# Kernel tuning notes

Hardware: AMD Instinct MI355X
Metric: run time of the kernel (lower is better)

## Reference

```python
import jax, jax.numpy as jnp
import numpy as np

B, S, HID = 2, 2048, 1024
NH, NKV, HD = 16, 8, 128
EPS = 1e-6
THETA = 1.0e6
NEG = -1e9

def _rope_tables():
    inv_freq = 1.0 / (THETA ** (np.arange(0, HD, 2, dtype=np.float32) / HD))  # [HD/2]
    pos = np.arange(S, dtype=np.float32)
    freqs = np.outer(pos, inv_freq)                      # [S, HD/2]
    emb = np.concatenate([freqs, freqs], axis=-1)        # [S, HD]
    cos = np.broadcast_to(np.cos(emb), (B, S, HD)).copy()
    sin = np.broadcast_to(np.sin(emb), (B, S, HD)).copy()
    return jnp.asarray(cos), jnp.asarray(sin)

def setup_inputs() -> dict:
    key = jax.random.key(0)
    ks = jax.random.split(key, 8)
    hidden_states = jax.random.normal(ks[0], (B, S, HID), jnp.float32)
    cos, sin = _rope_tables()
    # additive causal mask [B,1,S,S]
    causal = jnp.triu(jnp.full((S, S), NEG, jnp.float32), k=1)
    attention_mask = jnp.broadcast_to(causal[None, None], (B, 1, S, S))
    std = 0.02
    Wq = jax.random.normal(ks[1], (NH * HD, HID), jnp.float32) * std
    Wk = jax.random.normal(ks[2], (NKV * HD, HID), jnp.float32) * std
    Wv = jax.random.normal(ks[3], (NKV * HD, HID), jnp.float32) * std
    Wo = jax.random.normal(ks[4], (HID, NH * HD), jnp.float32) * std
    q_norm_w = jnp.ones((HD,), jnp.float32)
    k_norm_w = jnp.ones((HD,), jnp.float32)
    return {"hidden_states": hidden_states, "cos": cos, "sin": sin,
            "attention_mask": attention_mask, "Wq": Wq, "Wk": Wk, "Wv": Wv,
            "Wo": Wo, "q_norm_w": q_norm_w, "k_norm_w": k_norm_w}

def _rms_norm(x, w):
    var = jnp.mean(jnp.square(x), axis=-1, keepdims=True)
    return x * jax.lax.rsqrt(var + EPS) * w

def _rotate_half(x):
    x1, x2 = jnp.split(x, 2, axis=-1)
    return jnp.concatenate([-x2, x1], axis=-1)

def reference(hidden_states, cos, sin, attention_mask, Wq, Wk, Wv, Wo, q_norm_w, k_norm_w):
    # projections: [B,S,heads,HD] -> [B,heads,S,HD]
    q = jnp.einsum('bsh,dh->bsd', hidden_states, Wq).reshape(B, S, NH, HD)
    k = jnp.einsum('bsh,dh->bsd', hidden_states, Wk).reshape(B, S, NKV, HD)
    v = jnp.einsum('bsh,dh->bsd', hidden_states, Wv).reshape(B, S, NKV, HD)
    q = jnp.transpose(_rms_norm(q, q_norm_w), (0, 2, 1, 3))
    k = jnp.transpose(_rms_norm(k, k_norm_w), (0, 2, 1, 3))
    v = jnp.transpose(v, (0, 2, 1, 3))
    c = cos[:, None]  # [B,1,S,HD]
    s = sin[:, None]
    q = q * c + _rotate_half(q) * s
    k = k * c + _rotate_half(k) * s
    # repeat kv heads: NKV -> NH
    n_rep = NH // NKV
    k = jnp.repeat(k, n_rep, axis=1)
    v = jnp.repeat(v, n_rep, axis=1)
    scaling = HD ** -0.5
    scores = jnp.einsum('bhqd,bhkd->bhqk', q, k) * scaling
    scores = scores + attention_mask
    probs = jax.nn.softmax(scores.astype(jnp.float32), axis=-1).astype(q.dtype)
    out = jnp.einsum('bhqk,bhkd->bhqd', probs, v)
    out = jnp.transpose(out, (0, 2, 1, 3)).reshape(B, S, NH * HD)
    return jnp.einsum('bsd,hd->bsh', out, Wo)
```

## Files before the change

### kernel.cpp

```cpp
#include <hip/hip_runtime.h>
#include <hip/hip_fp16.h>


typedef _Float16 f16;
typedef __attribute__((ext_vector_type(8))) _Float16 f16x8;
typedef __attribute__((ext_vector_type(4))) _Float16 f16x4;
typedef __attribute__((ext_vector_type(4))) float f32x4;

__constant__ const float kEps = 1e-6f;
__constant__ const float kScaleL2 = 0.1275179120685481f;

#define ASYNC_LD16(gp, lp)                                              \
  __builtin_amdgcn_global_load_lds(                                     \
      (const __attribute__((address_space(1))) void*)(gp),              \
      (__attribute__((address_space(3))) void*)(uint32_t)(uintptr_t)(lp), 16, 0, 0)

__device__ __forceinline__ float dpp_max16(float v) {
  int x;
  x = __builtin_amdgcn_update_dpp(0, __builtin_bit_cast(int, v), 0xB1, 0xF, 0xF, true);
  v = fmaxf(v, __builtin_bit_cast(float, x));
  x = __builtin_amdgcn_update_dpp(0, __builtin_bit_cast(int, v), 0x4E, 0xF, 0xF, true);
  v = fmaxf(v, __builtin_bit_cast(float, x));
  x = __builtin_amdgcn_update_dpp(0, __builtin_bit_cast(int, v), 0x141, 0xF, 0xF, true);
  v = fmaxf(v, __builtin_bit_cast(float, x));
  x = __builtin_amdgcn_update_dpp(0, __builtin_bit_cast(int, v), 0x140, 0xF, 0xF, true);
  v = fmaxf(v, __builtin_bit_cast(float, x));
  return v;
}
__device__ __forceinline__ float dpp_sum16(float v) {
  int x;
  x = __builtin_amdgcn_update_dpp(0, __builtin_bit_cast(int, v), 0xB1, 0xF, 0xF, true);
  v += __builtin_bit_cast(float, x);
  x = __builtin_amdgcn_update_dpp(0, __builtin_bit_cast(int, v), 0x4E, 0xF, 0xF, true);
  v += __builtin_bit_cast(float, x);
  x = __builtin_amdgcn_update_dpp(0, __builtin_bit_cast(int, v), 0x141, 0xF, 0xF, true);
  v += __builtin_bit_cast(float, x);
  x = __builtin_amdgcn_update_dpp(0, __builtin_bit_cast(int, v), 0x140, 0xF, 0xF, true);
  v += __builtin_bit_cast(float, x);
  return v;
}

__global__ __launch_bounds__(256) void cast_f32_f16(const float* __restrict__ in,
                                                    f16* __restrict__ out, int n) {
  int i = (blockIdx.x * 256 + threadIdx.x) * 4;
  if (i >= n) return;
  f32x4 v = *reinterpret_cast<const f32x4*>(in + i);
  f16x4 o;
  o.x = (f16)v.x; o.y = (f16)v.y; o.z = (f16)v.z; o.w = (f16)v.w;
  *reinterpret_cast<f16x4*>(out + i) = o;
}

__global__ __launch_bounds__(256) void gemm_bt(const f16* __restrict__ A,
                                               const f16* __restrict__ Bm,
                                               float* __restrict__ C,
                                               int M, int N, int K) {
  __shared__ __align__(16) f16 As[128][64];
  __shared__ __align__(16) f16 Bs[128][64];
  const int tid = threadIdx.x;
  const int lane = tid & 63;
  const int wave = tid >> 6;
  const int cl = lane & 15;
  const int quad = lane >> 4;
  const int wm = (wave >> 1) * 64;
  const int wn = (wave & 1) * 64;
  const int tm = blockIdx.y * 128;
  const int tn = blockIdx.x * 128;
  const int r0 = tid >> 3;
  const int csw = ((tid & 7) ^ (r0 & 7)) * 8;

  const f16* Ab = A + (size_t)(tm + r0) * K + csw;
  const f16* Bb = Bm + (size_t)(tn + r0) * K + csw;
  char* Al = (char*)As + wave * 1024;
  char* Bl = (char*)Bs + wave * 1024;

  f32x4 acc[4][4] = {};

  for (int k0 = 0; k0 < K; k0 += 64) {
#pragma unroll
    for (int c = 0; c < 4; ++c) {
      ASYNC_LD16(Ab + (size_t)(c * 32) * K + k0, Al + c * 4096);
      ASYNC_LD16(Bb + (size_t)(c * 32) * K + k0, Bl + c * 4096);
    }
    __syncthreads();
#pragma unroll
    for (int kk = 0; kk < 2; ++kk) {
      f16x8 af[4], bf[4];
#pragma unroll
      for (int mi = 0; mi < 4; ++mi)
        af[mi] = *reinterpret_cast<const f16x8*>(
            &As[wm + mi * 16 + cl][((kk * 4 + quad) ^ (cl & 7)) * 8]);
#pragma unroll
      for (int ni = 0; ni < 4; ++ni)
        bf[ni] = *reinterpret_cast<const f16x8*>(
            &Bs[wn + ni * 16 + cl][((kk * 4 + quad) ^ (cl & 7)) * 8]);
#pragma unroll
      for (int mi = 0; mi < 4; ++mi)
#pragma unroll
        for (int ni = 0; ni < 4; ++ni)
          acc[mi][ni] =
              __builtin_amdgcn_mfma_f32_16x16x32_f16(af[mi], bf[ni], acc[mi][ni], 0, 0, 0);
    }
    __syncthreads();
  }
#pragma unroll
  for (int mi = 0; mi < 4; ++mi)
#pragma unroll
    for (int ni = 0; ni < 4; ++ni)
#pragma unroll
      for (int r = 0; r < 4; ++r)
        C[(size_t)(tm + wm + mi * 16 + quad * 4 + r) * N + tn + wn + ni * 16 + cl] =
            acc[mi][ni][r];
}

__global__ __launch_bounds__(256) void rope_norm(
    const float* __restrict__ qkvf,
    const float* __restrict__ cosT, const float* __restrict__ sinT,
    const float* __restrict__ qw, const float* __restrict__ kw,
    f16* __restrict__ qt, f16* __restrict__ kt) {
  const int gw = blockIdx.x * 4 + (threadIdx.x >> 6);
  const int lane = threadIdx.x & 63;
  const int head = gw % 24;
  const int bs = gw / 24;
  const bool isq = head < 16;
  const float* src = qkvf + (size_t)bs * 4096 +
                     (isq ? head * 128 : 2048 + (head - 16) * 128);
  const float x1 = src[lane];
  const float x2 = src[lane + 64];
  float ss = x1 * x1 + x2 * x2;
#pragma unroll
  for (int off = 32; off >= 1; off >>= 1) ss += __shfl_xor(ss, off);
  const float rms = rsqrtf(ss * (1.0f / 128.0f) + kEps);
  const float* w = isq ? qw : kw;
  const float n1 = x1 * rms * w[lane];
  const float n2 = x2 * rms * w[lane + 64];
  const float* cb = cosT + (size_t)bs * 128;
  const float* sb = sinT + (size_t)bs * 128;
  const float o1 = n1 * cb[lane] - n2 * sb[lane];
  const float o2 = n2 * cb[lane + 64] + n1 * sb[lane + 64];
  const int b = bs >> 11;
  const int s = bs & 2047;
  f16* dst;
  float sc;
  if (isq) {
    dst = qt + ((size_t)(b * 16 + head) * 2048 + s) * 128;
    sc = kScaleL2;
  } else {
    dst = kt + ((size_t)(b * 8 + (head - 16)) * 2048 + s) * 128;
    sc = 1.0f;
  }
  dst[lane] = (f16)(o1 * sc);
  dst[lane + 64] = (f16)(o2 * sc);
}

__global__ __launch_bounds__(256) void v_transpose(const float* __restrict__ qkvf,
                                                   f16* __restrict__ vt) {
  __shared__ f16 tile[64][136];
  const int bh = blockIdx.y;
  const int b = bh >> 3, h = bh & 7;
  const int s0 = blockIdx.x * 64;
  const int tid = threadIdx.x;
#pragma unroll
  for (int i = 0; i < 8; ++i) {
    int c = tid + i * 256;
    int s = c >> 5;
    int d0 = (c & 31) * 4;
    f32x4 v = *reinterpret_cast<const f32x4*>(
        qkvf + (size_t)(b * 2048 + s0 + s) * 4096 + 3072 + h * 128 + d0);
    tile[s][d0 + 0] = (f16)v.x;
    tile[s][d0 + 1] = (f16)v.y;
    tile[s][d0 + 2] = (f16)v.z;
    tile[s][d0 + 3] = (f16)v.w;
  }
  __syncthreads();
#pragma unroll
  for (int i = 0; i < 4; ++i) {
    int c = tid + i * 256;
    int d = c >> 3;
    int sB = (c & 7) * 8;
    f16x8 o;
#pragma unroll
    for (int j = 0; j < 8; ++j) o[j] = tile[sB + j][d];
    *reinterpret_cast<f16x8*>(vt + ((size_t)(b * 8 + h) * 128 + d) * 2048 + s0 + sB) = o;
  }
}

__global__ __launch_bounds__(128) void attn(const f16* __restrict__ Qt,
                                            const f16* __restrict__ Kt,
                                            const f16* __restrict__ Vt,
                                            f16* __restrict__ Ot) {
  __shared__ __align__(16) f16 Ks[64][136];
  __shared__ __align__(16) f16 Vs[128][72];
  __shared__ __align__(16) f16 Ps[2][32][72];

  const int bid = blockIdx.x;
  const int bh = bid & 31;
  const int t = 31 - (bid >> 5);
  const int q0 = t * 64;
  const int b = bh >> 4, h = bh & 15;
  const int kv = h >> 1;

  const int tid = threadIdx.x;
  const int lane = tid & 63, wv = tid >> 6;
  const int cl = lane & 15, quad = lane >> 4;

  const f16* qbase = Qt + ((size_t)(b * 16 + h) * 2048 + q0 + wv * 32 + cl) * 128;
  f16x8 aq[2][4];
#pragma unroll
  for (int mi = 0; mi < 2; ++mi)
#pragma unroll
    for (int kk = 0; kk < 4; ++kk)
      aq[mi][kk] =
          *reinterpret_cast<const f16x8*>(qbase + mi * 16 * 128 + kk * 32 + quad * 8);

  const f16* kbase = Kt + (size_t)(b * 8 + kv) * 2048 * 128;
  const f16* vbase = Vt + (size_t)(b * 8 + kv) * 128 * 2048;

  float m_[2][4], l_[2][4];
#pragma unroll
  for (int mi = 0; mi < 2; ++mi)
#pragma unroll
    for (int r = 0; r < 4; ++r) { m_[mi][r] = -1e30f; l_[mi][r] = 0.f; }
  f32x4 oacc[2][8] = {};

  for (int kt0 = 0; kt0 <= q0; kt0 += 64) {
#pragma unroll
    for (int i = 0; i < 8; ++i) {
      int c = tid + i * 128;
      int krow = c >> 4, d0 = (c & 15) * 8;
      *reinterpret_cast<int4*>(&Ks[krow][d0]) =
          *reinterpret_cast<const int4*>(kbase + (size_t)(kt0 + krow) * 128 + d0);
      int dr = c >> 3, ko = (c & 7) * 8;
      *reinterpret_cast<int4*>(&Vs[dr][ko]) =
          *reinterpret_cast<const int4*>(vbase + (size_t)dr * 2048 + kt0 + ko);
    }
    __syncthreads();
    f32x4 sacc[2][4] = {};
#pragma unroll
    for (int kk = 0; kk < 4; ++kk)
#pragma unroll
      for (int ni = 0; ni < 4; ++ni) {
        f16x8 bk = *reinterpret_cast<const f16x8*>(&Ks[ni * 16 + cl][kk * 32 + quad * 8]);
#pragma unroll
        for (int mi = 0; mi < 2; ++mi)
          sacc[mi][ni] =
              __builtin_amdgcn_mfma_f32_16x16x32_f16(aq[mi][kk], bk, sacc[mi][ni], 0, 0, 0);
      }
    if (kt0 == q0) {
#pragma unroll
      for (int mi = 0; mi < 2; ++mi) {
        const int qr = wv * 32 + mi * 16 + quad * 4;
#pragma unroll
        for (int ni = 0; ni < 4; ++ni) {
          const int kg = ni * 16 + cl;
#pragma unroll
          for (int r = 0; r < 4; ++r)
            if (kg > qr + r) sacc[mi][ni][r] = -1e30f;
        }
      }
    }
    float alv[2][4];
#pragma unroll
    for (int mi = 0; mi < 2; ++mi)
#pragma unroll
      for (int r = 0; r < 4; ++r) {
        float mx = fmaxf(fmaxf(sacc[mi][0][r], sacc[mi][1][r]),
                         fmaxf(sacc[mi][2][r], sacc[mi][3][r]));
        mx = dpp_max16(mx);
        const float nm = fmaxf(m_[mi][r], mx);
        const float al = __builtin_amdgcn_exp2f(m_[mi][r] - nm);
        m_[mi][r] = nm;
        float ps = 0.f;
#pragma unroll
        for (int ni = 0; ni < 4; ++ni) {
          const float p = __builtin_amdgcn_exp2f(sacc[mi][ni][r] - nm);
          sacc[mi][ni][r] = p;
          ps += p;
        }
        l_[mi][r] = l_[mi][r] * al + ps;
        alv[mi][r] = al;
      }
#pragma unroll
    for (int mi = 0; mi < 2; ++mi)
#pragma unroll
      for (int ni = 0; ni < 4; ++ni)
#pragma unroll
        for (int r = 0; r < 4; ++r)
          Ps[wv][mi * 16 + quad * 4 + r][ni * 16 + cl] = (f16)sacc[mi][ni][r];
#pragma unroll
    for (int mi = 0; mi < 2; ++mi)
#pragma unroll
      for (int dg = 0; dg < 8; ++dg)
#pragma unroll
        for (int r = 0; r < 4; ++r) oacc[mi][dg][r] *= alv[mi][r];
    asm volatile("s_waitcnt lgkmcnt(0)" ::: "memory");
    f16x8 ap[2][2];
#pragma unroll
    for (int mi = 0; mi < 2; ++mi)
#pragma unroll
      for (int kh = 0; kh < 2; ++kh)
        ap[mi][kh] =
            *reinterpret_cast<const f16x8*>(&Ps[wv][mi * 16 + cl][kh * 32 + quad * 8]);
#pragma unroll
    for (int kh = 0; kh < 2; ++kh)
#pragma unroll
      for (int dg = 0; dg < 8; ++dg) {
        f16x8 bv = *reinterpret_cast<const f16x8*>(&Vs[dg * 16 + cl][kh * 32 + quad * 8]);
#pragma unroll
        for (int mi = 0; mi < 2; ++mi)
          oacc[mi][dg] =
              __builtin_amdgcn_mfma_f32_16x16x32_f16(ap[mi][kh], bv, oacc[mi][dg], 0, 0, 0);
      }
    __syncthreads();
  }
#pragma unroll
  for (int mi = 0; mi < 2; ++mi)
#pragma unroll
    for (int r = 0; r < 4; ++r) {
      const float inv = 1.0f / dpp_sum16(l_[mi][r]);
      const int qg = q0 + wv * 32 + mi * 16 + quad * 4 + r;
#pragma unroll
      for (int dg = 0; dg < 8; ++dg)
        Ot[(size_t)(b * 2048 + qg) * 2048 + h * 128 + dg * 16 + cl] =
            (f16)(oacc[mi][dg][r] * inv);
    }
}

extern "C" void kernel_launch(void* const* d_in, const int* in_sizes, int n_in,
                              void* d_out, int out_size, void* d_ws, size_t ws_size,
                              hipStream_t stream) {
  (void)in_sizes; (void)n_in; (void)out_size; (void)ws_size;
  const float* hidden = (const float*)d_in[0];
  const float* cosT = (const float*)d_in[1];
  const float* sinT = (const float*)d_in[2];
  const float* Wq = (const float*)d_in[4];
  const float* Wk = (const float*)d_in[5];
  const float* Wv = (const float*)d_in[6];
  const float* Wo = (const float*)d_in[7];
  const float* qnw = (const float*)d_in[8];
  const float* knw = (const float*)d_in[9];
  float* out = (float*)d_out;

  char* ws = (char*)d_ws;
  size_t off = 0;
  auto alloc = [&](size_t bytes) {
    char* p = ws + off;
    off += (bytes + 255) & ~(size_t)255;
    return p;
  };
  f16* hb = (f16*)alloc(4096ull * 1024 * 2);
  f16* wqkv = (f16*)alloc(4096ull * 1024 * 2);
  f16* wob = (f16*)alloc(1024ull * 2048 * 2);
  float* qkvf = (float*)alloc(4096ull * 4096 * 4);
  f16* qt = (f16*)alloc(32ull * 2048 * 128 * 2);
  f16* kt = (f16*)alloc(16ull * 2048 * 128 * 2);
  f16* vt = (f16*)alloc(16ull * 2048 * 128 * 2);
  f16* ot = (f16*)alloc(4096ull * 2048 * 2);

  cast_f32_f16<<<4096, 256, 0, stream>>>(hidden, hb, 4194304);
  cast_f32_f16<<<2048, 256, 0, stream>>>(Wq, wqkv, 2097152);
  cast_f32_f16<<<1024, 256, 0, stream>>>(Wk, wqkv + 2048ull * 1024, 1048576);
  cast_f32_f16<<<1024, 256, 0, stream>>>(Wv, wqkv + 3072ull * 1024, 1048576);
  cast_f32_f16<<<2048, 256, 0, stream>>>(Wo, wob, 2097152);

  gemm_bt<<<dim3(32, 32), 256, 0, stream>>>(hb, wqkv, qkvf, 4096, 4096, 1024);

  rope_norm<<<24576, 256, 0, stream>>>(qkvf, cosT, sinT, qnw, knw, qt, kt);
  v_transpose<<<dim3(32, 16), 256, 0, stream>>>(qkvf, vt);

  attn<<<1024, 128, 0, stream>>>(qt, kt, vt, ot);

  gemm_bt<<<dim3(8, 32), 256, 0, stream>>>(ot, wob, out, 4096, 1024, 2048);
}
```

Measured before the change: 326.2 us.

## Restructure attention kernel with async double-buffered K/V and transposed MFMA layout

The attention kernel now uses 256-thread blocks covering 128 query rows, staging K/V tiles with async global-to-LDS loads into XOR-swizzled double buffers so the next tile loads while the current one computes. It computes S^T = K·Q^T so that probabilities stay in registers and feed the PV MFMA directly, which removes the Ps shared-memory round trip and the DPP row reductions. Causal tiles are scheduled in a balanced order, and masking is applied per wave. Register pressure goes up, and occupancy goes down because LDS use is larger.

Result: slower. 348.5 us (+6.9%).

```diff
diff --git a/kernel.cpp b/kernel.cpp
--- a/kernel.cpp
+++ b/kernel.cpp
@@ -14,31 +14,6 @@
   __builtin_amdgcn_global_load_lds(                                     \
       (const __attribute__((address_space(1))) void*)(gp),              \
       (__attribute__((address_space(3))) void*)(uint32_t)(uintptr_t)(lp), 16, 0, 0)
-
-__device__ __forceinline__ float dpp_max16(float v) {
-  int x;
-  x = __builtin_amdgcn_update_dpp(0, __builtin_bit_cast(int, v), 0xB1, 0xF, 0xF, true);
-  v = fmaxf(v, __builtin_bit_cast(float, x));
-  x = __builtin_amdgcn_update_dpp(0, __builtin_bit_cast(int, v), 0x4E, 0xF, 0xF, true);
-  v = fmaxf(v, __builtin_bit_cast(float, x));
-  x = __builtin_amdgcn_update_dpp(0, __builtin_bit_cast(int, v), 0x141, 0xF, 0xF, true);
-  v = fmaxf(v, __builtin_bit_cast(float, x));
-  x = __builtin_amdgcn_update_dpp(0, __builtin_bit_cast(int, v), 0x140, 0xF, 0xF, true);
-  v = fmaxf(v, __builtin_bit_cast(float, x));
-  return v;
-}
-__device__ __forceinline__ float dpp_sum16(float v) {
-  int x;
-  x = __builtin_amdgcn_update_dpp(0, __builtin_bit_cast(int, v), 0xB1, 0xF, 0xF, true);
-  v += __builtin_bit_cast(float, x);
-  x = __builtin_amdgcn_update_dpp(0, __builtin_bit_cast(int, v), 0x4E, 0xF, 0xF, true);
-  v += __builtin_bit_cast(float, x);
-  x = __builtin_amdgcn_update_dpp(0, __builtin_bit_cast(int, v), 0x141, 0xF, 0xF, true);
-  v += __builtin_bit_cast(float, x);
-  x = __builtin_amdgcn_update_dpp(0, __builtin_bit_cast(int, v), 0x140, 0xF, 0xF, true);
-  v += __builtin_bit_cast(float, x);
-  return v;
-}
 
 __global__ __launch_bounds__(256) void cast_f32_f16(const float* __restrict__ in,
                                                     f16* __restrict__ out, int n) {
@@ -184,18 +159,18 @@
   }
 }
 
-__global__ __launch_bounds__(128) void attn(const f16* __restrict__ Qt,
+__global__ __launch_bounds__(256) void attn(const f16* __restrict__ Qt,
                                             const f16* __restrict__ Kt,
                                             const f16* __restrict__ Vt,
                                             f16* __restrict__ Ot) {
-  __shared__ __align__(16) f16 Ks[64][136];
-  __shared__ __align__(16) f16 Vs[128][72];
-  __shared__ __align__(16) f16 Ps[2][32][72];
+  __shared__ __align__(16) f16 Kb[2][64 * 128];
+  __shared__ __align__(16) f16 Vb[2][128 * 64];
 
   const int bid = blockIdx.x;
+  const int group = bid >> 5;
+  const int t = (group < 8) ? (15 - group) : (group - 8);
   const int bh = bid & 31;
-  const int t = 31 - (bid >> 5);
-  const int q0 = t * 64;
+  const int q0 = t * 128;
   const int b = bh >> 4, h = bh & 15;
   const int kv = h >> 1;
 
@@ -215,114 +190,122 @@
   const f16* kbase = Kt + (size_t)(b * 8 + kv) * 2048 * 128;
   const f16* vbase = Vt + (size_t)(b * 8 + kv) * 128 * 2048;
 
-  float m_[2][4], l_[2][4];
-#pragma unroll
-  for (int mi = 0; mi < 2; ++mi)
-#pragma unroll
-    for (int r = 0; r < 4; ++r) { m_[mi][r] = -1e30f; l_[mi][r] = 0.f; }
-  f32x4 oacc[2][8] = {};
-
-  for (int kt0 = 0; kt0 <= q0; kt0 += 64) {
-#pragma unroll
-    for (int i = 0; i < 8; ++i) {
-      int c = tid + i * 128;
-      int krow = c >> 4, d0 = (c & 15) * 8;
-      *reinterpret_cast<int4*>(&Ks[krow][d0]) =
-          *reinterpret_cast<const int4*>(kbase + (size_t)(kt0 + krow) * 128 + d0);
-      int dr = c >> 3, ko = (c & 7) * 8;
-      *reinterpret_cast<int4*>(&Vs[dr][ko]) =
-          *reinterpret_cast<const int4*>(vbase + (size_t)dr * 2048 + kt0 + ko);
-    }
+  auto stage = [&](int kt0, int buf) {
+#pragma unroll
+    for (int cc = 0; cc < 4; ++cc) {
+      const int i = (wv * 4 + cc) * 64 + lane;
+      const int kr = i >> 4, ksc = i & 15;
+      const int kg = (ksc & 8) | ((ksc & 7) ^ (kr & 7));
+      ASYNC_LD16(kbase + (size_t)(kt0 + kr) * 128 + kg * 8,
+                 (char*)Kb[buf] + (wv * 4 + cc) * 1024);
+      const int vr = i >> 3, vsc = i & 7;
+      const int vg = vsc ^ (vr & 7);
+      ASYNC_LD16(vbase + (size_t)vr * 2048 + kt0 + vg * 8,
+                 (char*)Vb[buf] + (wv * 4 + cc) * 1024);
+    }
+  };
+
+  float m_[2], l_[2];
+#pragma unroll
+  for (int mi = 0; mi < 2; ++mi) { m_[mi] = -1e30f; l_[mi] = 0.f; }
+  f32x4 oacc[8][2] = {};
+
+  const int nIter = (q0 >> 6) + 2;
+  stage(0, 0);
+
+#pragma unroll 1
+  for (int it = 0; it < nIter; ++it) {
+    const int kt0 = it << 6;
     __syncthreads();
-    f32x4 sacc[2][4] = {};
+    if (it + 1 < nIter) stage(kt0 + 64, (it + 1) & 1);
+    const f16* Kc = Kb[it & 1];
+    const f16* Vc = Vb[it & 1];
+
+    f32x4 sacc[4][2] = {};
 #pragma unroll
     for (int kk = 0; kk < 4; ++kk)
 #pragma unroll
       for (int ni = 0; ni < 4; ++ni) {
-        f16x8 bk = *reinterpret_cast<const f16x8*>(&Ks[ni * 16 + cl][kk * 32 + quad * 8]);
+        const int sc = ((kk * 4 + quad) & 8) | (((kk * 4 + quad) & 7) ^ (cl & 7));
+        f16x8 ak = *reinterpret_cast<const f16x8*>(Kc + (ni * 16 + cl) * 128 + sc * 8);
 #pragma unroll
         for (int mi = 0; mi < 2; ++mi)
-          sacc[mi][ni] =
-              __builtin_amdgcn_mfma_f32_16x16x32_f16(aq[mi][kk], bk, sacc[mi][ni], 0, 0, 0);
+          sacc[ni][mi] =
+              __builtin_amdgcn_mfma_f32_16x16x32_f16(ak, aq[mi][kk], sacc[ni][mi], 0, 0, 0);
       }
-    if (kt0 == q0) {
-#pragma unroll
-      for (int mi = 0; mi < 2; ++mi) {
-        const int qr = wv * 32 + mi * 16 + quad * 4;
-#pragma unroll
-        for (int ni = 0; ni < 4; ++ni) {
-          const int kg = ni * 16 + cl;
+    if (kt0 + 64 > q0 + wv * 32) {
+#pragma unroll
+      for (int ni = 0; ni < 4; ++ni)
+#pragma unroll
+        for (int mi = 0; mi < 2; ++mi) {
+          const int qg = q0 + wv * 32 + mi * 16 + cl;
 #pragma unroll
           for (int r = 0; r < 4; ++r)
-            if (kg > qr + r) sacc[mi][ni][r] = -1e30f;
+            if (kt0 + ni * 16 + quad * 4 + r > qg) sacc[ni][mi][r] = -1e30f;
         }
-      }
-    }
-    float alv[2][4];
-#pragma unroll
-    for (int mi = 0; mi < 2; ++mi)
-#pragma unroll
-      for (int r = 0; r < 4; ++r) {
-        float mx = fmaxf(fmaxf(sacc[mi][0][r], sacc[mi][1][r]),
-                         fmaxf(sacc[mi][2][r], sacc[mi][3][r]));
-        mx = dpp_max16(mx);
-        const float nm = fmaxf(m_[mi][r], mx);
-        const float al = __builtin_amdgcn_exp2f(m_[mi][r] - nm);
-        m_[mi][r] = nm;
-        float ps = 0.f;
-#pragma unroll
-        for (int ni = 0; ni < 4; ++ni) {
-          const float p = __builtin_amdgcn_exp2f(sacc[mi][ni][r] - nm);
-          sacc[mi][ni][r] = p;
+    }
+    float al[2];
+#pragma unroll
+    for (int mi = 0; mi < 2; ++mi) {
+      float m0 = -1e30f;
+#pragma unroll
+      for (int ni = 0; ni < 4; ++ni)
+#pragma unroll
+        for (int r = 0; r < 4; ++r) m0 = fmaxf(m0, sacc[ni][mi][r]);
+      m0 = fmaxf(m0, __shfl_xor(m0, 16));
+      m0 = fmaxf(m0, __shfl_xor(m0, 32));
+      const float nm = fmaxf(m_[mi], m0);
+      al[mi] = __builtin_amdgcn_exp2f(m_[mi] - nm);
+      m_[mi] = nm;
+      float ps = 0.f;
+#pragma unroll
+      for (int ni = 0; ni < 4; ++ni)
+#pragma unroll
+        for (int r = 0; r < 4; ++r) {
+          const float p = __builtin_amdgcn_exp2f(sacc[ni][mi][r] - nm);
+          sacc[ni][mi][r] = p;
           ps += p;
         }
-        l_[mi][r] = l_[mi][r] * al + ps;
-        alv[mi][r] = al;
+      l_[mi] = l_[mi] * al[mi] + ps;
+    }
+    f16x4 pf[2][4];
+#pragma unroll
+    for (int mi = 0; mi < 2; ++mi)
+#pragma unroll
+      for (int ni = 0; ni < 4; ++ni)
+#pragma unroll
+        for (int r = 0; r < 4; ++r) pf[mi][ni][r] = (f16)sacc[ni][mi][r];
+#pragma unroll
+    for (int dblk = 0; dblk < 8; ++dblk)
+#pragma unroll
+      for (int mi = 0; mi < 2; ++mi) oacc[dblk][mi] *= al[mi];
+#pragma unroll
+    for (int s16 = 0; s16 < 4; ++s16)
+#pragma unroll
+      for (int dblk = 0; dblk < 8; ++dblk) {
+        const int vsc = ((s16 * 2 + (quad >> 1)) ^ (cl & 7));
+        f16x4 av = *reinterpret_cast<const f16x4*>(
+            Vc + (dblk * 16 + cl) * 64 + vsc * 8 + (quad & 1) * 4);
+#pragma unroll
+        for (int mi = 0; mi < 2; ++mi)
+          oacc[dblk][mi] =
+              __builtin_amdgcn_mfma_f32_16x16x16f16(av, pf[mi][s16], oacc[dblk][mi], 0, 0, 0);
       }
-#pragma unroll
-    for (int mi = 0; mi < 2; ++mi)
-#pragma unroll
-      for (int ni = 0; ni < 4; ++ni)
-#pragma unroll
-        for (int r = 0; r < 4; ++r)
-          Ps[wv][mi * 16 + quad * 4 + r][ni * 16 + cl] = (f16)sacc[mi][ni][r];
-#pragma unroll
-    for (int mi = 0; mi < 2; ++mi)
-#pragma unroll
-      for (int dg = 0; dg < 8; ++dg)
-#pragma unroll
-        for (int r = 0; r < 4; ++r) oacc[mi][dg][r] *= alv[mi][r];
-    asm volatile("s_waitcnt lgkmcnt(0)" ::: "memory");
-    f16x8 ap[2][2];
-#pragma unroll
-    for (int mi = 0; mi < 2; ++mi)
-#pragma unroll
-      for (int kh = 0; kh < 2; ++kh)
-        ap[mi][kh] =
-            *reinterpret_cast<const f16x8*>(&Ps[wv][mi * 16 + cl][kh * 32 + quad * 8]);
-#pragma unroll
-    for (int kh = 0; kh < 2; ++kh)
-#pragma unroll
-      for (int dg = 0; dg < 8; ++dg) {
-        f16x8 bv = *reinterpret_cast<const f16x8*>(&Vs[dg * 16 + cl][kh * 32 + quad * 8]);
-#pragma unroll
-        for (int mi = 0; mi < 2; ++mi)
-          oacc[mi][dg] =
-              __builtin_amdgcn_mfma_f32_16x16x32_f16(ap[mi][kh], bv, oacc[mi][dg], 0, 0, 0);
-      }
-    __syncthreads();
-  }
-#pragma unroll
-  for (int mi = 0; mi < 2; ++mi)
-#pragma unroll
-    for (int r = 0; r < 4; ++r) {
-      const float inv = 1.0f / dpp_sum16(l_[mi][r]);
-      const int qg = q0 + wv * 32 + mi * 16 + quad * 4 + r;
-#pragma unroll
-      for (int dg = 0; dg < 8; ++dg)
-        Ot[(size_t)(b * 2048 + qg) * 2048 + h * 128 + dg * 16 + cl] =
-            (f16)(oacc[mi][dg][r] * inv);
-    }
+  }
+#pragma unroll
+  for (int mi = 0; mi < 2; ++mi) {
+    l_[mi] += __shfl_xor(l_[mi], 16);
+    l_[mi] += __shfl_xor(l_[mi], 32);
+    const float inv = 1.0f / l_[mi];
+    const size_t qrow = (size_t)b * 2048 + q0 + wv * 32 + mi * 16 + cl;
+#pragma unroll
+    for (int dblk = 0; dblk < 8; ++dblk) {
+      f16x4 o;
+#pragma unroll
+      for (int r = 0; r < 4; ++r) o[r] = (f16)(oacc[dblk][mi][r] * inv);
+      *reinterpret_cast<f16x4*>(Ot + qrow * 2048 + h * 128 + dblk * 16 + quad * 4) = o;
+    }
+  }
 }
 
 extern "C" void kernel_launch(void* const* d_in, const int* in_sizes, int n_in,
@@ -367,7 +350,7 @@
   rope_norm<<<24576, 256, 0, stream>>>(qkvf, cosT, sinT, qnw, knw, qt, kt);
   v_transpose<<<dim3(32, 16), 256, 0, stream>>>(qkvf, vt);
 
-  attn<<<1024, 128, 0, stream>>>(qt, kt, vt, ot);
+  attn<<<512, 256, 0, stream>>>(qt, kt, vt, ot);
 
   gemm_bt<<<dim3(8, 32), 256, 0, stream>>>(ot, wob, out, 4096, 1024, 2048);
 }
```
